# Kernel optimization log

Measured on AMD Instinct MI355X. Metric: run time of the kernel, lower is better.

## Reference

```python
import jax, jax.numpy as jnp
import numpy as np

B, T, D, H, MLP, NI, OUT = 256, 2049, 64, 64, 128, 128, 10
L = D + D * (D - 1) // 2  # depth-2 logsignature channels = 2080


def _logsig_depth2(X, n_intervals):
    """Depth-2 log-signature of a piecewise-linear path over equal intervals.
    X: [B, T, D] with T = n_intervals*s + 1. Returns [B, n_intervals, L] where
    L = D + D(D-1)/2 (level-1 increments + strictly-upper-triangular Levy areas,
    the Lyndon-word basis signatory uses at depth 2)."""
    Bq, Tq, Dq = X.shape
    s = (Tq - 1) // n_intervals
    idx = np.arange(n_intervals)[:, None] * s + np.arange(s + 1)[None, :]
    seg = X[:, idx]                       # [B, n, s+1, D]
    inc = seg[:, :, -1] - seg[:, :, 0]    # level 1: [B, n, D]
    dlt = seg[:, :, 1:] - seg[:, :, :-1]  # per-step increments [B, n, s, D]
    cum = seg[:, :, :-1] - seg[:, :, :1]  # partial increments  [B, n, s, D]
    M = jnp.einsum('bnki,bnkj->bnij', cum, dlt)
    A = 0.5 * (M - jnp.swapaxes(M, -1, -2))  # Levy area [B, n, D, D]
    iu, ju = np.triu_indices(Dq, 1)
    return jnp.concatenate([inc, A[..., iu, ju]], axis=-1)  # [B, n, L]


def setup_inputs() -> dict:
    key = jax.random.key(0)
    ks = jax.random.split(key, 10)
    X = jax.random.normal(ks[0], (B, T, D), jnp.float32) * 0.05
    W_in = jax.random.normal(ks[1], (D, H), jnp.float32) / np.sqrt(D)
    b_in = jnp.zeros((H,), jnp.float32)
    W1 = jax.random.normal(ks[2], (H, MLP), jnp.float32) / np.sqrt(H)
    b1 = jnp.zeros((MLP,), jnp.float32)
    W2 = jax.random.normal(ks[3], (MLP, D * L), jnp.float32) / np.sqrt(MLP)
    b2 = jnp.zeros((D * L,), jnp.float32)
    W_out = jax.random.normal(ks[4], (H, OUT), jnp.float32) / np.sqrt(H)
    b_out = jnp.zeros((OUT,), jnp.float32)
    return {"X": X, "W_in": W_in, "b_in": b_in, "W1": W1, "b1": b1,
            "W2": W2, "b2": b2, "W_out": W_out, "b_out": b_out,
            "n_intervals": NI}


def reference(X, W_in, b_in, W1, b1, W2, b2, W_out, b_out, n_intervals):
    Bq, Tq, Dq = X.shape
    logsig = _logsig_depth2(X, n_intervals)        # [B, n, L]
    h0 = X[:, 0] @ W_in + b_in                     # initial_linear

    def vf(h):  # F.forward: MLP(h) -> [B, D, L]
        z = jnp.tanh(h @ W1 + b1)
        return (z @ W2 + b2).reshape(Bq, Dq, -1)

    def g(h, ls):  # f(h) contracted with logsig derivative
        return jnp.einsum('bdl,bl->bd', vf(h), ls)

    def rk4_step(h, ls):  # one RK4 step per interval, dt = 1
        k1 = g(h, ls)
        k2 = g(h + 0.5 * k1, ls)
        k3 = g(h + 0.5 * k2, ls)
        k4 = g(h + k3, ls)
        return h + (k1 + 2.0 * k2 + 2.0 * k3 + k4) / 6.0, None

    hT, _ = jax.lax.scan(rk4_step, h0, jnp.swapaxes(logsig, 0, 1))
    return hT @ W_out + b_out  # readout_linear: [B, OUT]
```

## Files before the change

### kernel.cpp

```cpp
#include <hip/hip_runtime.h>
#include <hip/hip_bf16.h>
#include <cstdint>
#include <cstddef>

#define B_SZ   256
#define T_SZ   2049
#define D_SZ   64
#define H_SZ   64
#define MLP_SZ 128
#define NI_SZ  128
#define SEG    16
#define KDIM   2080
#define KP     2112
#define OUT_SZ 10

#define NC     32
#define NCHUNK (NI_SZ / NC)
#define MROWS  (NC * B_SZ)
#define NB     8448
#define GSTR   8256
#define NT     (KP / 64)

typedef _Float16 f16x8 __attribute__((ext_vector_type(8)));
typedef float    f32x4 __attribute__((ext_vector_type(4)));

__device__ __forceinline__ float rlane(float v, int l) {
    return __uint_as_float(__builtin_amdgcn_readlane(__float_as_uint(v), l));
}

__global__ __launch_bounds__(256) void build_B(const float* __restrict__ W2,
                                               const float* __restrict__ b2,
                                               _Float16* __restrict__ Bm) {
    const int r = blockIdx.x, t = threadIdx.x;
    const float* src = nullptr;
    if (r < 8192) {
        const int d = r >> 7, m = r & 127;
        src = W2 + (size_t)m * (64 * KDIM) + (size_t)d * KDIM;
    } else if (r < 8256) {
        src = b2 + (size_t)(r - 8192) * KDIM;
    }
    _Float16* dst = Bm + (size_t)r * KP;
    for (int l = t; l < KP; l += 256)
        dst[l] = (src && l < KDIM) ? (_Float16)src[l] : (_Float16)0.0f;
}

__global__ void h0_kernel(const float* __restrict__ X, const float* __restrict__ W_in,
                          const float* __restrict__ b_in, float* __restrict__ h_state) {
    const int b = blockIdx.x, t = threadIdx.x;
    __shared__ float x0[D_SZ];
    if (t < D_SZ) x0[t] = X[(size_t)b * T_SZ * D_SZ + t];
    __syncthreads();
    float acc = b_in[t];
    for (int k = 0; k < D_SZ; ++k) acc += x0[k] * W_in[k * H_SZ + t];
    h_state[b * H_SZ + t] = acc;
}

__global__ __launch_bounds__(256) void logsig_kernel(const float* __restrict__ X,
                                                     _Float16* __restrict__ LS,
                                                     int n0) {
    const int b = blockIdx.x, sl = blockIdx.y, t = threadIdx.x;
    const int n = n0 + sl;
    __shared__ float seg[SEG + 1][D_SZ];
    __shared__ float cum[SEG][D_SZ];
    __shared__ float dlt[SEG][D_SZ];
    __shared__ float Mm[D_SZ][D_SZ + 1];

    const float* Xp = X + ((size_t)b * T_SZ + (size_t)n * SEG) * D_SZ;
    for (int i = t; i < (SEG + 1) * D_SZ / 4; i += 256)
        ((float4*)&seg[0][0])[i] = ((const float4*)Xp)[i];
    __syncthreads();
    for (int i = t; i < SEG * D_SZ; i += 256) {
        const int k = i >> 6, d = i & 63;
        cum[k][d] = seg[k][d] - seg[0][d];
        dlt[k][d] = seg[k + 1][d] - seg[k][d];
    }
    __syncthreads();

    const int ti = t >> 4, tj = t & 15;
    const int i0 = ti * 4, j0 = tj * 4;
    float m4[4][4] = {};
#pragma unroll
    for (int k = 0; k < SEG; ++k) {
        const float4 ci = *(const float4*)&cum[k][i0];
        const float4 dj = *(const float4*)&dlt[k][j0];
        const float* cip = (const float*)&ci;
        const float* djp = (const float*)&dj;
#pragma unroll
        for (int a = 0; a < 4; ++a)
#pragma unroll
            for (int c = 0; c < 4; ++c)
                m4[a][c] += cip[a] * djp[c];
    }
#pragma unroll
    for (int a = 0; a < 4; ++a)
#pragma unroll
        for (int c = 0; c < 4; ++c)
            Mm[i0 + a][j0 + c] = m4[a][c];
    __syncthreads();

    _Float16* out = LS + (size_t)(sl * B_SZ + b) * KP;
    if (t < D_SZ) out[t] = (_Float16)(seg[SEG][t] - seg[0][t]);
    if (t < KP - KDIM) out[KDIM + t] = (_Float16)0.0f;
    if (tj >= ti) {
#pragma unroll
        for (int a = 0; a < 4; ++a) {
            const int i = i0 + a;
#pragma unroll
            for (int c = 0; c < 4; ++c) {
                const int j = j0 + c;
                if (j > i) {
                    const int p = 63 * i - (i * (i - 1)) / 2 + (j - i - 1);
                    out[D_SZ + p] = (_Float16)(0.5f * (m4[a][c] - Mm[j][i]));
                }
            }
        }
    }
}

#define GLDS(SRC, DST) __builtin_amdgcn_global_load_lds(                        \
    (__attribute__((address_space(1))) void*)(SRC),                             \
    (__attribute__((address_space(3))) void*)(DST), 16, 0, 0)

#define STAGE(KT, KK, BUF) do {                                                 \
    const unsigned short* _sa = Asrc + (size_t)(KT) * 64 + (KK) * 32;           \
    const unsigned short* _sb = Bsrc + (size_t)(KT) * 64 + (KK) * 32;           \
    unsigned short* _d = ldst + (BUF) * 32768 + (KK) * 8192;                    \
    GLDS(_sa,                  _d);                                             \
    GLDS(_sa + (size_t)128*KP, _d + 4096);                                      \
    GLDS(_sb,                  _d + 16384);                                     \
    GLDS(_sb + (size_t)128*KP, _d + 20480);                                     \
} while (0)

#define BAR() do { __builtin_amdgcn_s_barrier(); __builtin_amdgcn_sched_barrier(0); } while (0)

#define VMW_(N) asm volatile("s_waitcnt vmcnt(" #N ")" ::: "memory")
#define VMW(N) VMW_(N)

#define LOAD_A(KK, MB) do {                                                     \
    af0 = *(const f16x8*)(aC + (KK) * 8192 + ((MB) + 0) * 512);                 \
    af1 = *(const f16x8*)(aC + (KK) * 8192 + ((MB) + 1) * 512);                 \
    af2 = *(const f16x8*)(aC + (KK) * 8192 + ((MB) + 2) * 512);                 \
    af3 = *(const f16x8*)(aC + (KK) * 8192 + ((MB) + 3) * 512);                 \
} while (0)

#define LOAD_B(KK) do {                                                         \
    bg0 = *(const f16x8*)(bC + (KK) * 8192 + 0 * 512);                          \
    bg1 = *(const f16x8*)(bC + (KK) * 8192 + 1 * 512);                          \
    bg2 = *(const f16x8*)(bC + (KK) * 8192 + 2 * 512);                          \
    bg3 = *(const f16x8*)(bC + (KK) * 8192 + 3 * 512);                          \
} while (0)

#define MFMA16(MB) do {                                                         \
    __builtin_amdgcn_s_setprio(1);                                              \
    acc[(MB)+0][0] = __builtin_amdgcn_mfma_f32_16x16x32_f16(af0, bg0, acc[(MB)+0][0], 0, 0, 0); \
    acc[(MB)+0][1] = __builtin_amdgcn_mfma_f32_16x16x32_f16(af0, bg1, acc[(MB)+0][1], 0, 0, 0); \
    acc[(MB)+1][0] = __builtin_amdgcn_mfma_f32_16x16x32_f16(af1, bg0, acc[(MB)+1][0], 0, 0, 0); \
    acc[(MB)+1][1] = __builtin_amdgcn_mfma_f32_16x16x32_f16(af1, bg1, acc[(MB)+1][1], 0, 0, 0); \
    acc[(MB)+0][2] = __builtin_amdgcn_mfma_f32_16x16x32_f16(af0, bg2, acc[(MB)+0][2], 0, 0, 0); \
    acc[(MB)+0][3] = __builtin_amdgcn_mfma_f32_16x16x32_f16(af0, bg3, acc[(MB)+0][3], 0, 0, 0); \
    acc[(MB)+1][2] = __builtin_amdgcn_mfma_f32_16x16x32_f16(af1, bg2, acc[(MB)+1][2], 0, 0, 0); \
    acc[(MB)+1][3] = __builtin_amdgcn_mfma_f32_16x16x32_f16(af1, bg3, acc[(MB)+1][3], 0, 0, 0); \
    acc[(MB)+2][0] = __builtin_amdgcn_mfma_f32_16x16x32_f16(af2, bg0, acc[(MB)+2][0], 0, 0, 0); \
    acc[(MB)+2][1] = __builtin_amdgcn_mfma_f32_16x16x32_f16(af2, bg1, acc[(MB)+2][1], 0, 0, 0); \
    acc[(MB)+3][0] = __builtin_amdgcn_mfma_f32_16x16x32_f16(af3, bg0, acc[(MB)+3][0], 0, 0, 0); \
    acc[(MB)+3][1] = __builtin_amdgcn_mfma_f32_16x16x32_f16(af3, bg1, acc[(MB)+3][1], 0, 0, 0); \
    acc[(MB)+2][2] = __builtin_amdgcn_mfma_f32_16x16x32_f16(af2, bg2, acc[(MB)+2][2], 0, 0, 0); \
    acc[(MB)+2][3] = __builtin_amdgcn_mfma_f32_16x16x32_f16(af2, bg3, acc[(MB)+2][3], 0, 0, 0); \
    acc[(MB)+3][2] = __builtin_amdgcn_mfma_f32_16x16x32_f16(af3, bg2, acc[(MB)+3][2], 0, 0, 0); \
    acc[(MB)+3][3] = __builtin_amdgcn_mfma_f32_16x16x32_f16(af3, bg3, acc[(MB)+3][3], 0, 0, 0); \
    __builtin_amdgcn_s_setprio(0);                                              \
} while (0)

#define TILE_BODY(TT, CUR, DOS1, DOS0, V1, V2) do {                             \
    const unsigned short* aC = aP + (CUR) * 32768;                              \
    const unsigned short* bC = bP + (CUR) * 32768;                              \
                                  \
    if (DOS1) { STAGE((TT) + 1, 1, (CUR) ^ 1); }                                \
    LOAD_B(0); LOAD_A(0, 0);                                                    \
    BAR(); MFMA16(0); BAR();                                                    \
                                                                        \
    LOAD_A(0, 4);                                                               \
    BAR(); MFMA16(4); VMW(V1); BAR();                                           \
                                    \
    if (DOS0) { STAGE((TT) + 2, 0, (CUR)); }                                    \
    LOAD_B(1); LOAD_A(1, 0);                                                    \
    BAR(); MFMA16(0); BAR();                                                    \
                                                                        \
    LOAD_A(1, 4);                                                               \
    BAR(); MFMA16(4); VMW(V2); BAR();                                           \
} while (0)

__global__ __launch_bounds__(512, 2) void gemm256(const unsigned short* __restrict__ A,
                                                  const unsigned short* __restrict__ Bm,
                                                  _Float16* __restrict__ C) {
    __shared__ unsigned short lds[65536];
    const int t = threadIdx.x;

    const int wg = blockIdx.x;
    const int x  = (wg & 7) * 132 + (wg >> 3);
    const int bx = x / 33, by = x % 33;
    const int tileM = bx * 256, tileN = by * 256;

    const int q7 = (t >> 3) & 7;
    const int u  = (t & 7) ^ q7;
    const int strow = ((t >> 3) << 1) + (u >> 2);
    const int stcol = (u & 3) << 3;
    const unsigned short* Asrc = A  + (size_t)(tileM + strow) * KP + stcol;
    const unsigned short* Bsrc = Bm + (size_t)(tileN + strow) * KP + stcol;
    unsigned short* ldst = lds + t * 8;

    const int lane = t & 63, w = t >> 6;
    const int wm = w >> 2, wn = w & 3;
    const int frow = lane & 15, j4 = lane >> 4;
    const int fr2 = frow >> 1;
    const int slot = (((frow & 1) << 2) | j4) ^ fr2;
    const unsigned short* aP = lds + wm * 4096 + fr2 * 64 + slot * 8;
    const unsigned short* bP = lds + 16384 + wn * 2048 + fr2 * 64 + slot * 8;

    f32x4 acc[8][4] = {};
    f16x8 af0, af1, af2, af3, bg0, bg1, bg2, bg3;

    STAGE(0, 0, 0);
    STAGE(0, 1, 0);
    STAGE(1, 0, 1);
    VMW(8);
    BAR();

    int cur = 0;
#pragma unroll 1
    for (int tt = 0; tt < NT - 2; ++tt) {
        TILE_BODY(tt, cur, 1, 1, 8, 8);
        cur ^= 1;
    }
    TILE_BODY(NT - 2, cur, 1, 0, 8, 4);
    cur ^= 1;
    TILE_BODY(NT - 1, cur, 0, 0, 0, 0);

    const int erow = j4 << 2;
#pragma unroll
    for (int mi = 0; mi < 8; ++mi) {
        const int grow = tileM + wm * 128 + mi * 16 + erow;
#pragma unroll
        for (int ni = 0; ni < 4; ++ni) {
            const int gcol = tileN + wn * 64 + ni * 16 + frow;
            if (gcol < GSTR) {
                _Float16* cp = C + (size_t)grow * GSTR + gcol;
#pragma unroll
                for (int r = 0; r < 4; ++r)
                    cp[(size_t)r * GSTR] = (_Float16)acc[mi][ni][r];
            }
        }
    }
}

__global__ __launch_bounds__(256) void ode_chunk(const _Float16* __restrict__ G,
                                                 const float* __restrict__ W1,
                                                 const float* __restrict__ b1,
                                                 float* __restrict__ h_state) {
    const int b = blockIdx.x, t = threadIdx.x;
    const int lane = t & 63, w = t >> 6;
    const int j0 = w * 32 + (lane & 31);
    __shared__ float ysw[4][D_SZ];
    __shared__ float part[2][4][D_SZ];

    float w1c[D_SZ];
#pragma unroll
    for (int dd = 0; dd < D_SZ; ++dd) w1c[dd] = W1[dd * MLP_SZ + j0];
    const float b1v = b1[j0];

    float hsv = h_state[b * H_SZ + lane];
    ysw[w][lane] = hsv;
    float k_st[4] = {0.f, 0.f, 0.f, 0.f};

    f16x8 pr[4];
    _Float16 b2pre;
    {
        const _Float16* Gr = G + (size_t)b * GSTR;
        const f16x8* gp = (const f16x8*)(Gr + lane * 128 + w * 32);
#pragma unroll
        for (int v = 0; v < 4; ++v) pr[v] = gp[v];
        b2pre = Gr[8192 + lane];
    }

#pragma unroll 1
    for (int s = 0; s < NC; ++s) {
        float gcur[32];
#pragma unroll
        for (int v = 0; v < 4; ++v)
#pragma unroll
            for (int e = 0; e < 8; ++e) gcur[v * 8 + e] = (float)pr[v][e];
        const float b2cur = (float)b2pre;
        if (s + 1 < NC) {
            const _Float16* Gr = G + (size_t)((s + 1) * B_SZ + b) * GSTR;
            const f16x8* gp = (const f16x8*)(Gr + lane * 128 + w * 32);
#pragma unroll
            for (int v = 0; v < 4; ++v) pr[v] = gp[v];
            b2pre = Gr[8192 + lane];
        }

#pragma unroll
        for (int st = 0; st < 4; ++st) {
            float a = 0.0f;
#pragma unroll
            for (int dd = 0; dd < D_SZ; dd += 4) {
                const float4 yv = *(const float4*)&ysw[w][dd];
                a += yv.x * w1c[dd] + yv.y * w1c[dd + 1]
                   + yv.z * w1c[dd + 2] + yv.w * w1c[dd + 3];
            }
            const float x = b1v + a;
            const float ex = __expf(2.0f * x);
            const float z = 1.0f - 2.0f / (ex + 1.0f);
            float a2 = 0.0f;
#pragma unroll
            for (int q = 0; q < 32; ++q)
                a2 += gcur[q] * rlane(z, q);
            part[st & 1][w][lane] = a2;
            __syncthreads();
            const float kv = b2cur + part[st & 1][0][lane] + part[st & 1][1][lane]
                           + part[st & 1][2][lane] + part[st & 1][3][lane];
            k_st[st] = kv;
            if (st < 3) {
                float y = hsv;
                if (st == 0) y += 0.5f * kv;
                else if (st == 1) y += 0.5f * kv;
                else y += kv;
                ysw[w][lane] = y;
            }
        }
        hsv += (k_st[0] + 2.0f * k_st[1] + 2.0f * k_st[2] + k_st[3]) * (1.0f / 6.0f);
        ysw[w][lane] = hsv;
    }
    if (w == 0) h_state[b * H_SZ + lane] = hsv;
}

__global__ void out_kernel(const float* __restrict__ h_state, const float* __restrict__ W_out,
                           const float* __restrict__ b_out, float* __restrict__ out) {
    const int b = blockIdx.x, t = threadIdx.x;
    __shared__ float hh[H_SZ];
    hh[t] = h_state[b * H_SZ + t];
    __syncthreads();
    if (t < OUT_SZ) {
        float acc = b_out[t];
        for (int d = 0; d < H_SZ; ++d) acc += hh[d] * W_out[d * OUT_SZ + t];
        out[b * OUT_SZ + t] = acc;
    }
}

extern "C" void kernel_launch(void* const* d_in, const int* in_sizes, int n_in,
                              void* d_out, int out_size, void* d_ws, size_t ws_size,
                              hipStream_t stream) {
    (void)in_sizes; (void)n_in; (void)out_size; (void)ws_size;
    const float* X     = (const float*)d_in[0];
    const float* W_in  = (const float*)d_in[1];
    const float* b_in  = (const float*)d_in[2];
    const float* W1    = (const float*)d_in[3];
    const float* b1    = (const float*)d_in[4];
    const float* W2    = (const float*)d_in[5];
    const float* b2    = (const float*)d_in[6];
    const float* W_out = (const float*)d_in[7];
    const float* b_out = (const float*)d_in[8];
    float* out = (float*)d_out;

    char* ws = (char*)d_ws;
    size_t off = 0;
    auto take = [&](size_t bytes) { void* p = ws + off; off = (off + bytes + 255) & ~(size_t)255; return p; };
    _Float16* Bmat = (_Float16*)take((size_t)NB * KP * 2);
    _Float16* LSc  = (_Float16*)take((size_t)MROWS * KP * 2);
    _Float16* G    = (_Float16*)take((size_t)MROWS * GSTR * 2);
    float*    hst  = (float*)take((size_t)B_SZ * H_SZ * 4);

    build_B<<<NB, 256, 0, stream>>>(W2, b2, Bmat);
    h0_kernel<<<B_SZ, H_SZ, 0, stream>>>(X, W_in, b_in, hst);

    for (int c = 0; c < NCHUNK; ++c) {
        logsig_kernel<<<dim3(B_SZ, NC), 256, 0, stream>>>(X, LSc, c * NC);
        gemm256<<<dim3(32 * 33), 512, 0, stream>>>(
            (const unsigned short*)LSc, (const unsigned short*)Bmat, G);
        ode_chunk<<<B_SZ, 256, 0, stream>>>(G, W1, b1, hst);
    }
    out_kernel<<<B_SZ, H_SZ, 0, stream>>>(hst, W_out, b_out, out);
}
```

Measured before the change: 1.987 ms.

## Switch GEMM to 32x32 MFMA, rebalance tail tile, split ODE reductions

The GEMM inner loop moves from 16x16x32 MFMA fragments to 32x32x16 MFMA, with new LDS fragment addressing and epilogue. The grid drops from 1056 to 1024 workgroups, and the leftover 33rd N-tile is handled as a second pass by the diagonal blocks, avoiding a small tail wave. The ODE kernel's serial dot-product chains are split into four independent accumulators to shorten dependency latency. The aim is fewer LDS reads per FLOP and better wave balance. The cost is some load imbalance on the 32 blocks that do two tiles.

```diff
diff --git a/kernel.cpp b/kernel.cpp
--- a/kernel.cpp
+++ b/kernel.cpp
@@ -23,6 +23,7 @@
 
 typedef _Float16 f16x8 __attribute__((ext_vector_type(8)));
 typedef float    f32x4 __attribute__((ext_vector_type(4)));
+typedef float    f32x16 __attribute__((ext_vector_type(16)));
 
 __device__ __forceinline__ float rlane(float v, int l) {
     return __uint_as_float(__builtin_amdgcn_readlane(__float_as_uint(v), l));
@@ -136,118 +137,118 @@
 #define VMW_(N) asm volatile("s_waitcnt vmcnt(" #N ")" ::: "memory")
 #define VMW(N) VMW_(N)
 
-#define LOAD_A(KK, MB) do {                                                     \
-    af0 = *(const f16x8*)(aC + (KK) * 8192 + ((MB) + 0) * 512);                 \
-    af1 = *(const f16x8*)(aC + (KK) * 8192 + ((MB) + 1) * 512);                 \
-    af2 = *(const f16x8*)(aC + (KK) * 8192 + ((MB) + 2) * 512);                 \
-    af3 = *(const f16x8*)(aC + (KK) * 8192 + ((MB) + 3) * 512);                 \
-} while (0)
-
-#define LOAD_B(KK) do {                                                         \
-    bg0 = *(const f16x8*)(bC + (KK) * 8192 + 0 * 512);                          \
-    bg1 = *(const f16x8*)(bC + (KK) * 8192 + 1 * 512);                          \
-    bg2 = *(const f16x8*)(bC + (KK) * 8192 + 2 * 512);                          \
-    bg3 = *(const f16x8*)(bC + (KK) * 8192 + 3 * 512);                          \
-} while (0)
-
-#define MFMA16(MB) do {                                                         \
+#define MFMA32(A, Bf, Cv) __builtin_amdgcn_mfma_f32_32x32x16_f16((A), (Bf), (Cv), 0, 0, 0)
+
+#define LDA(MH, KK) do {                                                        \
+    a0 = *(const f16x8*)(aC + (KK) * 8192 + (wm4 + (MH) * 2 + 0) * 1024 + fo);  \
+    a1 = *(const f16x8*)(aC + (KK) * 8192 + (wm4 + (MH) * 2 + 1) * 1024 + fo);  \
+    a2 = *(const f16x8*)(aC + (KK) * 8192 + (wm4 + (MH) * 2 + 0) * 1024 + (fo ^ 16)); \
+    a3 = *(const f16x8*)(aC + (KK) * 8192 + (wm4 + (MH) * 2 + 1) * 1024 + (fo ^ 16)); \
+} while (0)
+
+#define LDB(KK) do {                                                            \
+    b0 = *(const f16x8*)(bC + (KK) * 8192 + (wn2 + 0) * 1024 + fo);             \
+    b1 = *(const f16x8*)(bC + (KK) * 8192 + (wn2 + 1) * 1024 + fo);             \
+    b2 = *(const f16x8*)(bC + (KK) * 8192 + (wn2 + 0) * 1024 + (fo ^ 16));      \
+    b3 = *(const f16x8*)(bC + (KK) * 8192 + (wn2 + 1) * 1024 + (fo ^ 16));      \
+} while (0)
+
+#define MFMA8(MH) do {                                                          \
     __builtin_amdgcn_s_setprio(1);                                              \
-    acc[(MB)+0][0] = __builtin_amdgcn_mfma_f32_16x16x32_f16(af0, bg0, acc[(MB)+0][0], 0, 0, 0); \
-    acc[(MB)+0][1] = __builtin_amdgcn_mfma_f32_16x16x32_f16(af0, bg1, acc[(MB)+0][1], 0, 0, 0); \
-    acc[(MB)+1][0] = __builtin_amdgcn_mfma_f32_16x16x32_f16(af1, bg0, acc[(MB)+1][0], 0, 0, 0); \
-    acc[(MB)+1][1] = __builtin_amdgcn_mfma_f32_16x16x32_f16(af1, bg1, acc[(MB)+1][1], 0, 0, 0); \
-    acc[(MB)+0][2] = __builtin_amdgcn_mfma_f32_16x16x32_f16(af0, bg2, acc[(MB)+0][2], 0, 0, 0); \
-    acc[(MB)+0][3] = __builtin_amdgcn_mfma_f32_16x16x32_f16(af0, bg3, acc[(MB)+0][3], 0, 0, 0); \
-    acc[(MB)+1][2] = __builtin_amdgcn_mfma_f32_16x16x32_f16(af1, bg2, acc[(MB)+1][2], 0, 0, 0); \
-    acc[(MB)+1][3] = __builtin_amdgcn_mfma_f32_16x16x32_f16(af1, bg3, acc[(MB)+1][3], 0, 0, 0); \
-    acc[(MB)+2][0] = __builtin_amdgcn_mfma_f32_16x16x32_f16(af2, bg0, acc[(MB)+2][0], 0, 0, 0); \
-    acc[(MB)+2][1] = __builtin_amdgcn_mfma_f32_16x16x32_f16(af2, bg1, acc[(MB)+2][1], 0, 0, 0); \
-    acc[(MB)+3][0] = __builtin_amdgcn_mfma_f32_16x16x32_f16(af3, bg0, acc[(MB)+3][0], 0, 0, 0); \
-    acc[(MB)+3][1] = __builtin_amdgcn_mfma_f32_16x16x32_f16(af3, bg1, acc[(MB)+3][1], 0, 0, 0); \
-    acc[(MB)+2][2] = __builtin_amdgcn_mfma_f32_16x16x32_f16(af2, bg2, acc[(MB)+2][2], 0, 0, 0); \
-    acc[(MB)+2][3] = __builtin_amdgcn_mfma_f32_16x16x32_f16(af2, bg3, acc[(MB)+2][3], 0, 0, 0); \
-    acc[(MB)+3][2] = __builtin_amdgcn_mfma_f32_16x16x32_f16(af3, bg2, acc[(MB)+3][2], 0, 0, 0); \
-    acc[(MB)+3][3] = __builtin_amdgcn_mfma_f32_16x16x32_f16(af3, bg3, acc[(MB)+3][3], 0, 0, 0); \
+    acc[(MH)*2+0][0] = MFMA32(a0, b0, acc[(MH)*2+0][0]);                        \
+    acc[(MH)*2+0][1] = MFMA32(a0, b1, acc[(MH)*2+0][1]);                        \
+    acc[(MH)*2+1][0] = MFMA32(a1, b0, acc[(MH)*2+1][0]);                        \
+    acc[(MH)*2+1][1] = MFMA32(a1, b1, acc[(MH)*2+1][1]);                        \
+    acc[(MH)*2+0][0] = MFMA32(a2, b2, acc[(MH)*2+0][0]);                        \
+    acc[(MH)*2+0][1] = MFMA32(a2, b3, acc[(MH)*2+0][1]);                        \
+    acc[(MH)*2+1][0] = MFMA32(a3, b2, acc[(MH)*2+1][0]);                        \
+    acc[(MH)*2+1][1] = MFMA32(a3, b3, acc[(MH)*2+1][1]);                        \
     __builtin_amdgcn_s_setprio(0);                                              \
 } while (0)
 
 #define TILE_BODY(TT, CUR, DOS1, DOS0, V1, V2) do {                             \
-    const unsigned short* aC = aP + (CUR) * 32768;                              \
-    const unsigned short* bC = bP + (CUR) * 32768;                              \
+    const unsigned short* aC = ldsu + (CUR) * 32768;                            \
+    const unsigned short* bC = aC + 16384;                                      \
                                   \
     if (DOS1) { STAGE((TT) + 1, 1, (CUR) ^ 1); }                                \
-    LOAD_B(0); LOAD_A(0, 0);                                                    \
-    BAR(); MFMA16(0); BAR();                                                    \
+    LDB(0); LDA(0, 0);                                                          \
+    BAR(); MFMA8(0); BAR();                                                     \
                                                                         \
-    LOAD_A(0, 4);                                                               \
-    BAR(); MFMA16(4); VMW(V1); BAR();                                           \
+    LDA(1, 0);                                                                  \
+    BAR(); MFMA8(1); VMW(V1); BAR();                                            \
                                     \
     if (DOS0) { STAGE((TT) + 2, 0, (CUR)); }                                    \
-    LOAD_B(1); LOAD_A(1, 0);                                                    \
-    BAR(); MFMA16(0); BAR();                                                    \
+    LDB(1); LDA(0, 1);                                                          \
+    BAR(); MFMA8(0); BAR();                                                     \
                                                                         \
-    LOAD_A(1, 4);                                                               \
-    BAR(); MFMA16(4); VMW(V2); BAR();                                           \
+    LDA(1, 1);                                                                  \
+    BAR(); MFMA8(1); VMW(V2); BAR();                                            \
 } while (0)
 
 __global__ __launch_bounds__(512, 2) void gemm256(const unsigned short* __restrict__ A,
                                                   const unsigned short* __restrict__ Bm,
                                                   _Float16* __restrict__ C) {
-    __shared__ unsigned short lds[65536];
+    __shared__ __align__(16) unsigned short ldsu[65536];
     const int t = threadIdx.x;
 
     const int wg = blockIdx.x;
-    const int x  = (wg & 7) * 132 + (wg >> 3);
-    const int bx = x / 33, by = x % 33;
-    const int tileM = bx * 256, tileN = by * 256;
-
-    const int q7 = (t >> 3) & 7;
-    const int u  = (t & 7) ^ q7;
+    const int x  = (wg & 7) * 128 + (wg >> 3);
+    const int bx = x >> 5, by0 = x & 31;
+    const int nit = (by0 == bx) ? 2 : 1;
+    const int tileM = bx * 256;
+
+    const int q7s = (t >> 3) & 7;
+    const int u   = (t & 7) ^ q7s;
     const int strow = ((t >> 3) << 1) + (u >> 2);
     const int stcol = (u & 3) << 3;
-    const unsigned short* Asrc = A  + (size_t)(tileM + strow) * KP + stcol;
-    const unsigned short* Bsrc = Bm + (size_t)(tileN + strow) * KP + stcol;
-    unsigned short* ldst = lds + t * 8;
+    const unsigned short* Asrc = A + (size_t)(tileM + strow) * KP + stcol;
+    unsigned short* ldst = ldsu + t * 8;
 
     const int lane = t & 63, w = t >> 6;
     const int wm = w >> 2, wn = w & 3;
-    const int frow = lane & 15, j4 = lane >> 4;
-    const int fr2 = frow >> 1;
-    const int slot = (((frow & 1) << 2) | j4) ^ fr2;
-    const unsigned short* aP = lds + wm * 4096 + fr2 * 64 + slot * 8;
-    const unsigned short* bP = lds + 16384 + wn * 2048 + fr2 * 64 + slot * 8;
-
-    f32x4 acc[8][4] = {};
-    f16x8 af0, af1, af2, af3, bg0, bg1, bg2, bg3;
-
-    STAGE(0, 0, 0);
-    STAGE(0, 1, 0);
-    STAGE(1, 0, 1);
-    VMW(8);
-    BAR();
-
-    int cur = 0;
+    const int wm4 = wm * 4, wn2 = wn * 2;
+    const int lrow = lane & 31, cc = lane >> 5;
+    const int ql = lrow >> 1, pp = lrow & 1;
+    const int fo = ql * 64 + ((((pp << 2) | cc) ^ (ql & 7)) << 3);
+
 #pragma unroll 1
-    for (int tt = 0; tt < NT - 2; ++tt) {
-        TILE_BODY(tt, cur, 1, 1, 8, 8);
+    for (int it = 0; it < nit; ++it) {
+        const int tileN = (it == 0 ? by0 : 32) * 256;
+        const unsigned short* Bsrc = Bm + (size_t)(tileN + strow) * KP + stcol;
+
+        f32x16 acc[4][2] = {};
+        f16x8 a0, a1, a2, a3, b0, b1, b2, b3;
+
+        STAGE(0, 0, 0);
+        STAGE(0, 1, 0);
+        STAGE(1, 0, 1);
+        VMW(8);
+        BAR();
+
+        int cur = 0;
+#pragma unroll 1
+        for (int tt = 0; tt < NT - 2; ++tt) {
+            TILE_BODY(tt, cur, 1, 1, 8, 8);
+            cur ^= 1;
+        }
+        TILE_BODY(NT - 2, cur, 1, 0, 8, 4);
         cur ^= 1;
-    }
-    TILE_BODY(NT - 2, cur, 1, 0, 8, 4);
-    cur ^= 1;
-    TILE_BODY(NT - 1, cur, 0, 0, 0, 0);
-
-    const int erow = j4 << 2;
-#pragma unroll
-    for (int mi = 0; mi < 8; ++mi) {
-        const int grow = tileM + wm * 128 + mi * 16 + erow;
-#pragma unroll
-        for (int ni = 0; ni < 4; ++ni) {
-            const int gcol = tileN + wn * 64 + ni * 16 + frow;
-            if (gcol < GSTR) {
-                _Float16* cp = C + (size_t)grow * GSTR + gcol;
-#pragma unroll
-                for (int r = 0; r < 4; ++r)
-                    cp[(size_t)r * GSTR] = (_Float16)acc[mi][ni][r];
+        TILE_BODY(NT - 1, cur, 0, 0, 0, 0);
+
+#pragma unroll
+        for (int rb = 0; rb < 4; ++rb) {
+            const int rbase = tileM + wm * 128 + rb * 32 + cc * 4;
+#pragma unroll
+            for (int cb = 0; cb < 2; ++cb) {
+                const int col = tileN + wn * 64 + cb * 32 + lrow;
+                if (col < GSTR) {
+#pragma unroll
+                    for (int rg = 0; rg < 4; ++rg)
+#pragma unroll
+                        for (int rr = 0; rr < 4; ++rr)
+                            C[(size_t)(rbase + rg * 8 + rr) * GSTR + col] =
+                                (_Float16)acc[rb][cb][rg * 4 + rr];
+                }
             }
         }
     }
@@ -300,21 +301,27 @@
 
 #pragma unroll
         for (int st = 0; st < 4; ++st) {
-            float a = 0.0f;
+            float ax = 0.f, ay = 0.f, az = 0.f, aw = 0.f;
 #pragma unroll
             for (int dd = 0; dd < D_SZ; dd += 4) {
                 const float4 yv = *(const float4*)&ysw[w][dd];
-                a += yv.x * w1c[dd] + yv.y * w1c[dd + 1]
-                   + yv.z * w1c[dd + 2] + yv.w * w1c[dd + 3];
-            }
-            const float x = b1v + a;
-            const float ex = __expf(2.0f * x);
+                ax += yv.x * w1c[dd];
+                ay += yv.y * w1c[dd + 1];
+                az += yv.z * w1c[dd + 2];
+                aw += yv.w * w1c[dd + 3];
+            }
+            const float xx = b1v + ((ax + ay) + (az + aw));
+            const float ex = __expf(2.0f * xx);
             const float z = 1.0f - 2.0f / (ex + 1.0f);
-            float a2 = 0.0f;
-#pragma unroll
-            for (int q = 0; q < 32; ++q)
-                a2 += gcur[q] * rlane(z, q);
-            part[st & 1][w][lane] = a2;
+            float s0 = 0.f, s1 = 0.f, s2 = 0.f, s3 = 0.f;
+#pragma unroll
+            for (int q = 0; q < 32; q += 4) {
+                s0 += gcur[q]     * rlane(z, q);
+                s1 += gcur[q + 1] * rlane(z, q + 1);
+                s2 += gcur[q + 2] * rlane(z, q + 2);
+                s3 += gcur[q + 3] * rlane(z, q + 3);
+            }
+            part[st & 1][w][lane] = (s0 + s1) + (s2 + s3);
             __syncthreads();
             const float kv = b2cur + part[st & 1][0][lane] + part[st & 1][1][lane]
                            + part[st & 1][2][lane] + part[st & 1][3][lane];
@@ -374,7 +381,7 @@
 
     for (int c = 0; c < NCHUNK; ++c) {
         logsig_kernel<<<dim3(B_SZ, NC), 256, 0, stream>>>(X, LSc, c * NC);
-        gemm256<<<dim3(32 * 33), 512, 0, stream>>>(
+        gemm256<<<dim3(1024), 512, 0, stream>>>(
             (const unsigned short*)LSc, (const unsigned short*)Bmat, G);
         ode_chunk<<<B_SZ, 256, 0, stream>>>(G, W1, b1, hst);
     }
```

After: 2.803 ms. +41.0%, slower.

## Rebalance GEMM tiles to 1024 blocks and split ODE dot-product accumulators

Applied to the files above, without the earlier changes.

The GEMM grid drops from 1056 tile blocks to 1024. The first 32 blocks now compute two N-tiles each: their diagonal tile plus the last, mostly padded column tile 32. The other blocks handle one off-diagonal tile each, which is meant to even out the tail wave on the 256-CU device. The ODE kernel's two inner dot products now use four independent accumulators to shorten the dependent FMA chains. This reorders the floating-point sums slightly, and the 32 double-duty blocks lengthen the critical path for those blocks.

```diff
diff --git a/kernel.cpp b/kernel.cpp
--- a/kernel.cpp
+++ b/kernel.cpp
@@ -193,20 +193,29 @@
 __global__ __launch_bounds__(512, 2) void gemm256(const unsigned short* __restrict__ A,
                                                   const unsigned short* __restrict__ Bm,
                                                   _Float16* __restrict__ C) {
-    __shared__ unsigned short lds[65536];
+    __shared__ __align__(16) unsigned short lds[65536];
     const int t = threadIdx.x;
 
     const int wg = blockIdx.x;
-    const int x  = (wg & 7) * 132 + (wg >> 3);
-    const int bx = x / 33, by = x % 33;
-    const int tileM = bx * 256, tileN = by * 256;
-
-    const int q7 = (t >> 3) & 7;
-    const int u  = (t & 7) ^ q7;
+    int bx, by0, nit;
+    if (wg < 32) {
+        bx = (wg & 7) * 4 + (wg >> 3);
+        by0 = bx;
+        nit = 2;
+    } else {
+        const int idx = (wg - 32) >> 3;
+        bx = (wg & 7) * 4 + idx / 31;
+        const int byi = idx % 31;
+        by0 = byi + (byi >= bx ? 1 : 0);
+        nit = 1;
+    }
+    const int tileM = bx * 256;
+
+    const int q7s = (t >> 3) & 7;
+    const int u   = (t & 7) ^ q7s;
     const int strow = ((t >> 3) << 1) + (u >> 2);
     const int stcol = (u & 3) << 3;
-    const unsigned short* Asrc = A  + (size_t)(tileM + strow) * KP + stcol;
-    const unsigned short* Bsrc = Bm + (size_t)(tileN + strow) * KP + stcol;
+    const unsigned short* Asrc = A + (size_t)(tileM + strow) * KP + stcol;
     unsigned short* ldst = lds + t * 8;
 
     const int lane = t & 63, w = t >> 6;
@@ -217,37 +226,43 @@
     const unsigned short* aP = lds + wm * 4096 + fr2 * 64 + slot * 8;
     const unsigned short* bP = lds + 16384 + wn * 2048 + fr2 * 64 + slot * 8;
 
-    f32x4 acc[8][4] = {};
-    f16x8 af0, af1, af2, af3, bg0, bg1, bg2, bg3;
-
-    STAGE(0, 0, 0);
-    STAGE(0, 1, 0);
-    STAGE(1, 0, 1);
-    VMW(8);
-    BAR();
-
-    int cur = 0;
 #pragma unroll 1
-    for (int tt = 0; tt < NT - 2; ++tt) {
-        TILE_BODY(tt, cur, 1, 1, 8, 8);
+    for (int it = 0; it < nit; ++it) {
+        const int tileN = (it == 0 ? by0 : 32) * 256;
+        const unsigned short* Bsrc = Bm + (size_t)(tileN + strow) * KP + stcol;
+
+        f32x4 acc[8][4] = {};
+        f16x8 af0, af1, af2, af3, bg0, bg1, bg2, bg3;
+
+        STAGE(0, 0, 0);
+        STAGE(0, 1, 0);
+        STAGE(1, 0, 1);
+        VMW(8);
+        BAR();
+
+        int cur = 0;
+#pragma unroll 1
+        for (int tt = 0; tt < NT - 2; ++tt) {
+            TILE_BODY(tt, cur, 1, 1, 8, 8);
+            cur ^= 1;
+        }
+        TILE_BODY(NT - 2, cur, 1, 0, 8, 4);
         cur ^= 1;
-    }
-    TILE_BODY(NT - 2, cur, 1, 0, 8, 4);
-    cur ^= 1;
-    TILE_BODY(NT - 1, cur, 0, 0, 0, 0);
-
-    const int erow = j4 << 2;
-#pragma unroll
-    for (int mi = 0; mi < 8; ++mi) {
-        const int grow = tileM + wm * 128 + mi * 16 + erow;
-#pragma unroll
-        for (int ni = 0; ni < 4; ++ni) {
-            const int gcol = tileN + wn * 64 + ni * 16 + frow;
-            if (gcol < GSTR) {
-                _Float16* cp = C + (size_t)grow * GSTR + gcol;
-#pragma unroll
-                for (int r = 0; r < 4; ++r)
-                    cp[(size_t)r * GSTR] = (_Float16)acc[mi][ni][r];
+        TILE_BODY(NT - 1, cur, 0, 0, 0, 0);
+
+        const int erow = j4 << 2;
+#pragma unroll
+        for (int mi = 0; mi < 8; ++mi) {
+            const int grow = tileM + wm * 128 + mi * 16 + erow;
+#pragma unroll
+            for (int ni = 0; ni < 4; ++ni) {
+                const int gcol = tileN + wn * 64 + ni * 16 + frow;
+                if (gcol < GSTR) {
+                    _Float16* cp = C + (size_t)grow * GSTR + gcol;
+#pragma unroll
+                    for (int r = 0; r < 4; ++r)
+                        cp[(size_t)r * GSTR] = (_Float16)acc[mi][ni][r];
+                }
             }
         }
     }
@@ -300,21 +315,27 @@
 
 #pragma unroll
         for (int st = 0; st < 4; ++st) {
-            float a = 0.0f;
+            float ax = 0.f, ay = 0.f, az = 0.f, aw = 0.f;
 #pragma unroll
             for (int dd = 0; dd < D_SZ; dd += 4) {
                 const float4 yv = *(const float4*)&ysw[w][dd];
-                a += yv.x * w1c[dd] + yv.y * w1c[dd + 1]
-                   + yv.z * w1c[dd + 2] + yv.w * w1c[dd + 3];
+                ax += yv.x * w1c[dd];
+                ay += yv.y * w1c[dd + 1];
+                az += yv.z * w1c[dd + 2];
+                aw += yv.w * w1c[dd + 3];
             }
-            const float x = b1v + a;
-            const float ex = __expf(2.0f * x);
+            const float xx = b1v + ((ax + ay) + (az + aw));
+            const float ex = __expf(2.0f * xx);
             const float z = 1.0f - 2.0f / (ex + 1.0f);
-            float a2 = 0.0f;
-#pragma unroll
-            for (int q = 0; q < 32; ++q)
-                a2 += gcur[q] * rlane(z, q);
-            part[st & 1][w][lane] = a2;
+            float s0 = 0.f, s1 = 0.f, s2 = 0.f, s3 = 0.f;
+#pragma unroll
+            for (int q = 0; q < 32; q += 4) {
+                s0 += gcur[q]     * rlane(z, q);
+                s1 += gcur[q + 1] * rlane(z, q + 1);
+                s2 += gcur[q + 2] * rlane(z, q + 2);
+                s3 += gcur[q + 3] * rlane(z, q + 3);
+            }
+            part[st & 1][w][lane] = (s0 + s1) + (s2 + s3);
             __syncthreads();
             const float kv = b2cur + part[st & 1][0][lane] + part[st & 1][1][lane]
                            + part[st & 1][2][lane] + part[st & 1][3][lane];
@@ -374,7 +395,7 @@
 
     for (int c = 0; c < NCHUNK; ++c) {
         logsig_kernel<<<dim3(B_SZ, NC), 256, 0, stream>>>(X, LSc, c * NC);
-        gemm256<<<dim3(32 * 33), 512, 0, stream>>>(
+        gemm256<<<dim3(1024), 512, 0, stream>>>(
             (const unsigned short*)LSc, (const unsigned short*)Bmat, G);
         ode_chunk<<<B_SZ, 256, 0, stream>>>(G, W1, b1, hst);
     }
```

New measurement: 2.072 ms. 1.04x slower.
